# Kernel tuning notes

Measured on AMD Instinct MI355X. Metric: run time of the kernel, lower is better.

Reference implementation:

```python
import jax, jax.numpy as jnp
import numpy as np

B, IN, H = 4096, 1024, 1024


def setup_inputs() -> dict:
    key = jax.random.key(0)
    ks = jax.random.split(key, 16)
    s = 1.0 / np.sqrt(IN)
    inp = {
        "x_t": jax.random.normal(ks[0], (B, IN), jnp.float32),
        "h_prev": jax.random.normal(ks[1], (B, H), jnp.float32),
        "c_prev": jax.random.normal(ks[2], (B, H), jnp.float32),
        "W_xi": jax.random.uniform(ks[3], (H, IN), jnp.float32, -s, s),
        "W_hi": jax.random.normal(ks[4], (H, H), jnp.float32) / np.sqrt(H),
        "b_i": jnp.zeros((H,), jnp.float32),
        "W_xf": jax.random.uniform(ks[5], (H, IN), jnp.float32, -s, s),
        "W_hf": jax.random.normal(ks[6], (H, H), jnp.float32) / np.sqrt(H),
        "b_f": jnp.ones((H,), jnp.float32),
        "W_xg": jax.random.uniform(ks[7], (H, IN), jnp.float32, -s, s),
        "W_hg": jax.random.normal(ks[8], (H, H), jnp.float32) / np.sqrt(H),
        "b_g": jnp.zeros((H,), jnp.float32),
        "W_xo": jax.random.uniform(ks[9], (H, IN), jnp.float32, -s, s),
        "W_ho": jax.random.normal(ks[10], (H, H), jnp.float32) / np.sqrt(H),
        "b_o": jnp.zeros((H,), jnp.float32),
    }
    return inp


def reference(x_t, h_prev, c_prev,
              W_xi, W_hi, b_i,
              W_xf, W_hf, b_f,
              W_xg, W_hg, b_g,
              W_xo, W_ho, b_o):
    # i/f/g/o gates: sigmoid/sigmoid/tanh/sigmoid of (x W_x^T + h W_h^T + b)
    i_t = jax.nn.sigmoid(x_t @ W_xi.T + h_prev @ W_hi.T + b_i)
    f_t = jax.nn.sigmoid(x_t @ W_xf.T + h_prev @ W_hf.T + b_f)
    g_t = jnp.tanh(x_t @ W_xg.T + h_prev @ W_hg.T + b_g)
    o_t = jax.nn.sigmoid(x_t @ W_xo.T + h_prev @ W_ho.T + b_o)
    c_t = f_t * c_prev + i_t * g_t
    h_t = o_t * jnp.tanh(c_t)
    return (h_t, c_t)
```

## Files before the change

kernel.cpp:

```cpp
#include <hip/hip_runtime.h>
#include <hip/hip_bf16.h>


constexpr int Mdim = 4096;
constexpr int Ndim = 4096;
constexpr int Kdim = 2048;
constexpr int Hdim = 1024;
constexpr int BM = 256;
constexpr int BN = 256;
constexpr int BK = 64;
constexpr int NT = Kdim / BK;

using short8 = __attribute__((ext_vector_type(8))) short;
using f32x4  = __attribute__((ext_vector_type(4))) float;

__device__ __forceinline__ float sigmoid_(float x) {
    return 1.f / (1.f + __expf(-x));
}
__device__ __forceinline__ float tanh_(float x) {
    float e = __expf(2.f * x);
    return (e - 1.f) / (e + 1.f);
}

__global__ void build_A(const float* __restrict__ x, const float* __restrict__ h,
                        __hip_bfloat16* __restrict__ A) {
    int idx = blockIdx.x * 256 + threadIdx.x;
    int row = idx >> 8;
    int c8  = (idx & 255) * 8;
    const float* src = (c8 < 1024) ? (x + (size_t)row * 1024 + c8)
                                   : (h + (size_t)row * 1024 + (c8 - 1024));
    float4 f0 = ((const float4*)src)[0];
    float4 f1 = ((const float4*)src)[1];
    union { short8 v; __hip_bfloat16 e[8]; } u;
    u.e[0] = __float2bfloat16(f0.x); u.e[1] = __float2bfloat16(f0.y);
    u.e[2] = __float2bfloat16(f0.z); u.e[3] = __float2bfloat16(f0.w);
    u.e[4] = __float2bfloat16(f1.x); u.e[5] = __float2bfloat16(f1.y);
    u.e[6] = __float2bfloat16(f1.z); u.e[7] = __float2bfloat16(f1.w);
    *(short8*)(A + (size_t)row * Kdim + c8) = u.v;
}

__global__ void build_B(const float* __restrict__ Wxi, const float* __restrict__ Whi,
                        const float* __restrict__ Wxf, const float* __restrict__ Whf,
                        const float* __restrict__ Wxg, const float* __restrict__ Whg,
                        const float* __restrict__ Wxo, const float* __restrict__ Who,
                        __hip_bfloat16* __restrict__ B) {
    int idx = blockIdx.x * 256 + threadIdx.x;
    int n  = idx >> 8;
    int c8 = (idx & 255) * 8;
    int g = (n >> 4) & 3;
    int j = ((n >> 6) << 4) | (n & 15);
    const float* Wx = (g == 0) ? Wxi : (g == 1) ? Wxf : (g == 2) ? Wxg : Wxo;
    const float* Wh = (g == 0) ? Whi : (g == 1) ? Whf : (g == 2) ? Whg : Who;
    const float* src = (c8 < 1024) ? (Wx + (size_t)j * 1024 + c8)
                                   : (Wh + (size_t)j * 1024 + (c8 - 1024));
    float4 f0 = ((const float4*)src)[0];
    float4 f1 = ((const float4*)src)[1];
    union { short8 v; __hip_bfloat16 e[8]; } u;
    u.e[0] = __float2bfloat16(f0.x); u.e[1] = __float2bfloat16(f0.y);
    u.e[2] = __float2bfloat16(f0.z); u.e[3] = __float2bfloat16(f0.w);
    u.e[4] = __float2bfloat16(f1.x); u.e[5] = __float2bfloat16(f1.y);
    u.e[6] = __float2bfloat16(f1.z); u.e[7] = __float2bfloat16(f1.w);
    *(short8*)(B + (size_t)n * Kdim + c8) = u.v;
}

#define RD(p) (*(const short8*)(p))

__launch_bounds__(512, 1)
__global__ void lstm_gemm(const __hip_bfloat16* __restrict__ A,
                          const __hip_bfloat16* __restrict__ B,
                          const float* __restrict__ c_prev,
                          const float* __restrict__ b_i, const float* __restrict__ b_f,
                          const float* __restrict__ b_g, const float* __restrict__ b_o,
                          float* __restrict__ out_h, float* __restrict__ out_c) {
    __shared__ __hip_bfloat16 lds[2][2][2][128 * 64];

    const int tid  = threadIdx.x;
    const int lane = tid & 63;
    const int w    = tid >> 6;
    const int wr   = w >> 2;
    const int wc   = w & 3;
    const int l15  = lane & 15, lhi = lane >> 4;

    int bid = blockIdx.x;
    int swz = (bid & 7) * 32 + (bid >> 3);
    const int bm = (swz >> 4) * BM;
    const int bn = (swz & 15) * BN;

    const int srow_  = tid >> 3;
    const int schunk = ((tid & 7) ^ ((tid >> 3) & 7)) * 8;

    const int swz4 = (l15 & 7) << 4;
    const int kof0 = (lhi * 16) ^ swz4;
    const int kof1 = (64 + lhi * 16) ^ swz4;

#define STG1(dstbase, byteoff, srcptr, grow, kcol)                              \
    __builtin_amdgcn_global_load_lds(                                           \
        (const __attribute__((address_space(1))) unsigned*)(                    \
            (srcptr) + (size_t)((grow) + srow_) * Kdim + (kcol) + schunk),      \
        (__attribute__((address_space(3))) unsigned*)(                          \
            (char*)(dstbase) + (byteoff) + tid * 16), 16, 0, 0)

#define STAGE_TILE(s, kc)                                                       \
    do {                                                                        \
        STG1(&lds[s][1][0][0], 0,    B, bn + 0,   kc);                          \
        STG1(&lds[s][1][0][0], 8192, B, bn + 64,  kc);                          \
        STG1(&lds[s][1][1][0], 0,    B, bn + 128, kc);                          \
        STG1(&lds[s][1][1][0], 8192, B, bn + 192, kc);                          \
        STG1(&lds[s][0][0][0], 0,    A, bm + 0,   kc);                          \
        STG1(&lds[s][0][0][0], 8192, A, bm + 64,  kc);                          \
        STG1(&lds[s][0][1][0], 0,    A, bm + 128, kc);                          \
        STG1(&lds[s][0][1][0], 8192, A, bm + 192, kc);                          \
    } while (0)

    f32x4 acc[8][4];
#pragma unroll
    for (int a = 0; a < 8; ++a)
#pragma unroll
        for (int b = 0; b < 4; ++b)
            acc[a][b] = (f32x4){0.f, 0.f, 0.f, 0.f};

    STAGE_TILE(0, 0);
    __builtin_amdgcn_sched_barrier(0);
    asm volatile("s_waitcnt vmcnt(0)" ::: "memory");
    __builtin_amdgcn_s_barrier();

    for (int t = 0; t < NT; ++t) {
        const int d = t & 1;

        if (t + 1 < NT) STAGE_TILE(d ^ 1, (t + 1) * BK);

        const char* Ab = (const char*)&lds[d][0][wr][0] + l15 * 128;
        const char* Bb = (const char*)&lds[d][1][wc >> 1][0] + ((wc & 1) * 64 + l15) * 128;

        short8 af[8][2], bf[4][2];
#pragma unroll
        for (int a = 0; a < 8; ++a) {
            af[a][0] = RD(Ab + a * 2048 + kof0);
            af[a][1] = RD(Ab + a * 2048 + kof1);
        }
#pragma unroll
        for (int b = 0; b < 4; ++b) {
            bf[b][0] = RD(Bb + b * 2048 + kof0);
            bf[b][1] = RD(Bb + b * 2048 + kof1);
        }

        __builtin_amdgcn_s_setprio(1);
#pragma unroll
        for (int a = 0; a < 8; ++a)
#pragma unroll
            for (int b = 0; b < 4; ++b)
#pragma unroll
                for (int kk = 0; kk < 2; ++kk)
                    acc[a][b] = __builtin_amdgcn_mfma_f32_16x16x32_bf16(
                        af[a][kk], bf[b][kk], acc[a][b], 0, 0, 0);
        __builtin_amdgcn_s_setprio(0);

        if (t + 1 < NT) {
            __builtin_amdgcn_sched_barrier(0);
            asm volatile("s_waitcnt vmcnt(0) lgkmcnt(0)" ::: "memory");
            __builtin_amdgcn_s_barrier();
        }
    }
#undef STG1
#undef STAGE_TILE

    const int j0 = ((bn + wc * 64) >> 6) * 16 + l15;
    const float bi  = b_i[j0];
    const float bf_ = b_f[j0];
    const float bg  = b_g[j0];
    const float bo  = b_o[j0];

#pragma unroll
    for (int a = 0; a < 8; ++a) {
        int mbase = bm + wr * 128 + a * 16 + lhi * 4;
#pragma unroll
        for (int r = 0; r < 4; ++r) {
            int m = mbase + r;
            float vi = acc[a][0][r] + bi;
            float vf = acc[a][1][r] + bf_;
            float vg = acc[a][2][r] + bg;
            float vo = acc[a][3][r] + bo;
            float it = sigmoid_(vi);
            float ft = sigmoid_(vf);
            float gt = tanh_(vg);
            float ot = sigmoid_(vo);
            float cp = c_prev[(size_t)m * Hdim + j0];
            float ct = ft * cp + it * gt;
            float ht = ot * tanh_(ct);
            out_h[(size_t)m * Hdim + j0] = ht;
            out_c[(size_t)m * Hdim + j0] = ct;
        }
    }
}

extern "C" void kernel_launch(void* const* d_in, const int* in_sizes, int n_in,
                              void* d_out, int out_size, void* d_ws, size_t ws_size,
                              hipStream_t stream) {
    const float* x_t    = (const float*)d_in[0];
    const float* h_prev = (const float*)d_in[1];
    const float* c_prev = (const float*)d_in[2];
    const float* W_xi   = (const float*)d_in[3];
    const float* W_hi   = (const float*)d_in[4];
    const float* b_i    = (const float*)d_in[5];
    const float* W_xf   = (const float*)d_in[6];
    const float* W_hf   = (const float*)d_in[7];
    const float* b_f    = (const float*)d_in[8];
    const float* W_xg   = (const float*)d_in[9];
    const float* W_hg   = (const float*)d_in[10];
    const float* b_g    = (const float*)d_in[11];
    const float* W_xo   = (const float*)d_in[12];
    const float* W_ho   = (const float*)d_in[13];
    const float* b_o    = (const float*)d_in[14];

    float* out_h = (float*)d_out;
    float* out_c = out_h + (size_t)Mdim * Hdim;

    __hip_bfloat16* Abf = (__hip_bfloat16*)d_ws;
    __hip_bfloat16* Bbf = Abf + (size_t)Mdim * Kdim;

    build_A<<<4096, 256, 0, stream>>>(x_t, h_prev, Abf);
    build_B<<<4096, 256, 0, stream>>>(W_xi, W_hi, W_xf, W_hf, W_xg, W_hg, W_xo, W_ho, Bbf);

    lstm_gemm<<<dim3((Mdim / BM) * (Ndim / BN)), 512, 0, stream>>>(
        Abf, Bbf, c_prev, b_i, b_f, b_g, b_o, out_h, out_c);
}
```

Baseline: 86.34 us.

## Load B fragments directly from global into registers, halve LDS for two blocks/CU

```diff
diff --git a/kernel.cpp b/kernel.cpp
--- a/kernel.cpp
+++ b/kernel.cpp
@@ -65,14 +65,14 @@
 
 #define RD(p) (*(const short8*)(p))
 
-__launch_bounds__(512, 1)
+__launch_bounds__(512, 2)
 __global__ void lstm_gemm(const __hip_bfloat16* __restrict__ A,
                           const __hip_bfloat16* __restrict__ B,
                           const float* __restrict__ c_prev,
                           const float* __restrict__ b_i, const float* __restrict__ b_f,
                           const float* __restrict__ b_g, const float* __restrict__ b_o,
                           float* __restrict__ out_h, float* __restrict__ out_c) {
-    __shared__ __hip_bfloat16 lds[2][2][2][128 * 64];
+    __shared__ __hip_bfloat16 lds[2][2][128 * 64];
 
     const int tid  = threadIdx.x;
     const int lane = tid & 63;
@@ -93,23 +93,59 @@
     const int kof0 = (lhi * 16) ^ swz4;
     const int kof1 = (64 + lhi * 16) ^ swz4;
 
-#define STG1(dstbase, byteoff, srcptr, grow, kcol)                              \
+    const __hip_bfloat16* bRow = B + (size_t)(bn + wc * 64 + l15) * Kdim + lhi * 8;
+
+#define STG1(dstbase, byteoff, grow, kcol)                                      \
     __builtin_amdgcn_global_load_lds(                                           \
         (const __attribute__((address_space(1))) unsigned*)(                    \
-            (srcptr) + (size_t)((grow) + srow_) * Kdim + (kcol) + schunk),      \
+            A + (size_t)((grow) + srow_) * Kdim + (kcol) + schunk),             \
         (__attribute__((address_space(3))) unsigned*)(                          \
             (char*)(dstbase) + (byteoff) + tid * 16), 16, 0, 0)
 
-#define STAGE_TILE(s, kc)                                                       \
+#define STAGE_A(s, kc)                                                          \
     do {                                                                        \
-        STG1(&lds[s][1][0][0], 0,    B, bn + 0,   kc);                          \
-        STG1(&lds[s][1][0][0], 8192, B, bn + 64,  kc);                          \
-        STG1(&lds[s][1][1][0], 0,    B, bn + 128, kc);                          \
-        STG1(&lds[s][1][1][0], 8192, B, bn + 192, kc);                          \
-        STG1(&lds[s][0][0][0], 0,    A, bm + 0,   kc);                          \
-        STG1(&lds[s][0][0][0], 8192, A, bm + 64,  kc);                          \
-        STG1(&lds[s][0][1][0], 0,    A, bm + 128, kc);                          \
-        STG1(&lds[s][0][1][0], 8192, A, bm + 192, kc);                          \
+        STG1(&lds[s][0][0], 0,    bm + 0,   kc);                                \
+        STG1(&lds[s][0][0], 8192, bm + 64,  kc);                                \
+        STG1(&lds[s][1][0], 0,    bm + 128, kc);                                \
+        STG1(&lds[s][1][0], 8192, bm + 192, kc);                                \
+    } while (0)
+
+#define LOAD_B(dst, kt_)                                                        \
+    do {                                                                        \
+        _Pragma("unroll")                                                       \
+        for (int b_ = 0; b_ < 4; ++b_) {                                        \
+            dst[b_][0] = RD(bRow + (size_t)b_ * 16 * Kdim + (kt_));             \
+            dst[b_][1] = RD(bRow + (size_t)b_ * 16 * Kdim + (kt_) + 32);        \
+        }                                                                       \
+    } while (0)
+
+#define TILE_BODY(t_, dcur, BC, BN_)                                            \
+    do {                                                                        \
+        const int hasNext = (t_) + 1 < NT;                                      \
+        if (hasNext) {                                                          \
+            LOAD_B(BN_, ((t_) + 1) * BK);                                       \
+            STAGE_A(dcur ^ 1, ((t_) + 1) * BK);                                 \
+        }                                                                       \
+        const char* Ab = (const char*)&lds[dcur][wr][0] + l15 * 128;            \
+        __builtin_amdgcn_s_setprio(1);                                          \
+        _Pragma("unroll")                                                       \
+        for (int a = 0; a < 8; ++a) {                                           \
+            short8 af0 = RD(Ab + a * 2048 + kof0);                              \
+            short8 af1 = RD(Ab + a * 2048 + kof1);                              \
+            _Pragma("unroll")                                                   \
+            for (int b = 0; b < 4; ++b) {                                       \
+                acc[a][b] = __builtin_amdgcn_mfma_f32_16x16x32_bf16(            \
+                    af0, BC[b][0], acc[a][b], 0, 0, 0);                         \
+                acc[a][b] = __builtin_amdgcn_mfma_f32_16x16x32_bf16(            \
+                    af1, BC[b][1], acc[a][b], 0, 0, 0);                         \
+            }                                                                   \
+        }                                                                       \
+        __builtin_amdgcn_s_setprio(0);                                          \
+        if (hasNext) {                                                          \
+            __builtin_amdgcn_sched_barrier(0);                                  \
+            asm volatile("s_waitcnt vmcnt(0) lgkmcnt(0)" ::: "memory");         \
+            __builtin_amdgcn_s_barrier();                                       \
+        }                                                                       \
     } while (0)
 
     f32x4 acc[8][4];
@@ -119,50 +155,22 @@
         for (int b = 0; b < 4; ++b)
             acc[a][b] = (f32x4){0.f, 0.f, 0.f, 0.f};
 
-    STAGE_TILE(0, 0);
+    short8 bfA[4][2], bfB[4][2];
+
+    STAGE_A(0, 0);
+    LOAD_B(bfA, 0);
     __builtin_amdgcn_sched_barrier(0);
     asm volatile("s_waitcnt vmcnt(0)" ::: "memory");
     __builtin_amdgcn_s_barrier();
 
-    for (int t = 0; t < NT; ++t) {
-        const int d = t & 1;
-
-        if (t + 1 < NT) STAGE_TILE(d ^ 1, (t + 1) * BK);
-
-        const char* Ab = (const char*)&lds[d][0][wr][0] + l15 * 128;
-        const char* Bb = (const char*)&lds[d][1][wc >> 1][0] + ((wc & 1) * 64 + l15) * 128;
-
-        short8 af[8][2], bf[4][2];
-#pragma unroll
-        for (int a = 0; a < 8; ++a) {
-            af[a][0] = RD(Ab + a * 2048 + kof0);
-            af[a][1] = RD(Ab + a * 2048 + kof1);
-        }
-#pragma unroll
-        for (int b = 0; b < 4; ++b) {
-            bf[b][0] = RD(Bb + b * 2048 + kof0);
-            bf[b][1] = RD(Bb + b * 2048 + kof1);
-        }
-
-        __builtin_amdgcn_s_setprio(1);
-#pragma unroll
-        for (int a = 0; a < 8; ++a)
-#pragma unroll
-            for (int b = 0; b < 4; ++b)
-#pragma unroll
-                for (int kk = 0; kk < 2; ++kk)
-                    acc[a][b] = __builtin_amdgcn_mfma_f32_16x16x32_bf16(
-                        af[a][kk], bf[b][kk], acc[a][b], 0, 0, 0);
-        __builtin_amdgcn_s_setprio(0);
-
-        if (t + 1 < NT) {
-            __builtin_amdgcn_sched_barrier(0);
-            asm volatile("s_waitcnt vmcnt(0) lgkmcnt(0)" ::: "memory");
-            __builtin_amdgcn_s_barrier();
-        }
+    for (int tt = 0; tt < NT; tt += 2) {
+        TILE_BODY(tt,     0, bfA, bfB);
+        TILE_BODY(tt + 1, 1, bfB, bfA);
     }
 #undef STG1
-#undef STAGE_TILE
+#undef STAGE_A
+#undef LOAD_B
+#undef TILE_BODY
 
     const int j0 = ((bn + wc * 64) >> 6) * 16 + l15;
     const float bi  = b_i[j0];
```

After: 118.8 us. 37.6% more time.

## Shrink GEMM tile to 128x256, single-buffer LDS, raise occupancy to several blocks per CU

Applied to the files above, without the earlier changes.

```diff
diff --git a/kernel.cpp b/kernel.cpp
--- a/kernel.cpp
+++ b/kernel.cpp
@@ -6,7 +6,7 @@
 constexpr int Ndim = 4096;
 constexpr int Kdim = 2048;
 constexpr int Hdim = 1024;
-constexpr int BM = 256;
+constexpr int BM = 128;
 constexpr int BN = 256;
 constexpr int BK = 64;
 constexpr int NT = Kdim / BK;
@@ -65,14 +65,15 @@
 
 #define RD(p) (*(const short8*)(p))
 
-__launch_bounds__(512, 1)
+__launch_bounds__(512, 4)
 __global__ void lstm_gemm(const __hip_bfloat16* __restrict__ A,
                           const __hip_bfloat16* __restrict__ B,
                           const float* __restrict__ c_prev,
                           const float* __restrict__ b_i, const float* __restrict__ b_f,
                           const float* __restrict__ b_g, const float* __restrict__ b_o,
                           float* __restrict__ out_h, float* __restrict__ out_c) {
-    __shared__ __hip_bfloat16 lds[2][2][2][128 * 64];
+    __shared__ __hip_bfloat16 As[128 * 64];
+    __shared__ __hip_bfloat16 Bs[256 * 64];
 
     const int tid  = threadIdx.x;
     const int lane = tid & 63;
@@ -82,7 +83,7 @@
     const int l15  = lane & 15, lhi = lane >> 4;
 
     int bid = blockIdx.x;
-    int swz = (bid & 7) * 32 + (bid >> 3);
+    int swz = (bid & 7) * 64 + (bid >> 3);
     const int bm = (swz >> 4) * BM;
     const int bn = (swz & 15) * BN;
 
@@ -90,8 +91,6 @@
     const int schunk = ((tid & 7) ^ ((tid >> 3) & 7)) * 8;
 
     const int swz4 = (l15 & 7) << 4;
-    const int kof0 = (lhi * 16) ^ swz4;
-    const int kof1 = (64 + lhi * 16) ^ swz4;
 
 #define STG1(dstbase, byteoff, srcptr, grow, kcol)                              \
     __builtin_amdgcn_global_load_lds(                                           \
@@ -100,64 +99,54 @@
         (__attribute__((address_space(3))) unsigned*)(                          \
             (char*)(dstbase) + (byteoff) + tid * 16), 16, 0, 0)
 
-#define STAGE_TILE(s, kc)                                                       \
+#define STAGE_TILE(kc)                                                          \
     do {                                                                        \
-        STG1(&lds[s][1][0][0], 0,    B, bn + 0,   kc);                          \
-        STG1(&lds[s][1][0][0], 8192, B, bn + 64,  kc);                          \
-        STG1(&lds[s][1][1][0], 0,    B, bn + 128, kc);                          \
-        STG1(&lds[s][1][1][0], 8192, B, bn + 192, kc);                          \
-        STG1(&lds[s][0][0][0], 0,    A, bm + 0,   kc);                          \
-        STG1(&lds[s][0][0][0], 8192, A, bm + 64,  kc);                          \
-        STG1(&lds[s][0][1][0], 0,    A, bm + 128, kc);                          \
-        STG1(&lds[s][0][1][0], 8192, A, bm + 192, kc);                          \
+        STG1(As, 0,     A, bm + 0,   kc);                                       \
+        STG1(As, 8192,  A, bm + 64,  kc);                                       \
+        STG1(Bs, 0,     B, bn + 0,   kc);                                       \
+        STG1(Bs, 8192,  B, bn + 64,  kc);                                       \
+        STG1(Bs, 16384, B, bn + 128, kc);                                       \
+        STG1(Bs, 24576, B, bn + 192, kc);                                       \
     } while (0)
 
-    f32x4 acc[8][4];
-#pragma unroll
-    for (int a = 0; a < 8; ++a)
+    f32x4 acc[4][4];
+#pragma unroll
+    for (int a = 0; a < 4; ++a)
 #pragma unroll
         for (int b = 0; b < 4; ++b)
             acc[a][b] = (f32x4){0.f, 0.f, 0.f, 0.f};
 
-    STAGE_TILE(0, 0);
+    STAGE_TILE(0);
     __builtin_amdgcn_sched_barrier(0);
     asm volatile("s_waitcnt vmcnt(0)" ::: "memory");
     __builtin_amdgcn_s_barrier();
 
     for (int t = 0; t < NT; ++t) {
-        const int d = t & 1;
-
-        if (t + 1 < NT) STAGE_TILE(d ^ 1, (t + 1) * BK);
-
-        const char* Ab = (const char*)&lds[d][0][wr][0] + l15 * 128;
-        const char* Bb = (const char*)&lds[d][1][wc >> 1][0] + ((wc & 1) * 64 + l15) * 128;
-
-        short8 af[8][2], bf[4][2];
-#pragma unroll
-        for (int a = 0; a < 8; ++a) {
-            af[a][0] = RD(Ab + a * 2048 + kof0);
-            af[a][1] = RD(Ab + a * 2048 + kof1);
+#pragma unroll
+        for (int kk = 0; kk < 2; ++kk) {
+            const int kof = (kk * 64 + lhi * 16) ^ swz4;
+            short8 af[4], bf[4];
+#pragma unroll
+            for (int a = 0; a < 4; ++a)
+                af[a] = RD((const char*)As + (wr * 64 + a * 16 + l15) * 128 + kof);
+#pragma unroll
+            for (int b = 0; b < 4; ++b)
+                bf[b] = RD((const char*)Bs + (wc * 64 + b * 16 + l15) * 128 + kof);
+            __builtin_amdgcn_s_setprio(1);
+#pragma unroll
+            for (int a = 0; a < 4; ++a)
+#pragma unroll
+                for (int b = 0; b < 4; ++b)
+                    acc[a][b] = __builtin_amdgcn_mfma_f32_16x16x32_bf16(
+                        af[a], bf[b], acc[a][b], 0, 0, 0);
+            __builtin_amdgcn_s_setprio(0);
         }
-#pragma unroll
-        for (int b = 0; b < 4; ++b) {
-            bf[b][0] = RD(Bb + b * 2048 + kof0);
-            bf[b][1] = RD(Bb + b * 2048 + kof1);
-        }
-
-        __builtin_amdgcn_s_setprio(1);
-#pragma unroll
-        for (int a = 0; a < 8; ++a)
-#pragma unroll
-            for (int b = 0; b < 4; ++b)
-#pragma unroll
-                for (int kk = 0; kk < 2; ++kk)
-                    acc[a][b] = __builtin_amdgcn_mfma_f32_16x16x32_bf16(
-                        af[a][kk], bf[b][kk], acc[a][b], 0, 0, 0);
-        __builtin_amdgcn_s_setprio(0);
 
         if (t + 1 < NT) {
+            __builtin_amdgcn_s_barrier();
+            STAGE_TILE((t + 1) * BK);
             __builtin_amdgcn_sched_barrier(0);
-            asm volatile("s_waitcnt vmcnt(0) lgkmcnt(0)" ::: "memory");
+            asm volatile("s_waitcnt vmcnt(0)" ::: "memory");
             __builtin_amdgcn_s_barrier();
         }
     }
@@ -171,8 +160,8 @@
     const float bo  = b_o[j0];
 
 #pragma unroll
-    for (int a = 0; a < 8; ++a) {
-        int mbase = bm + wr * 128 + a * 16 + lhi * 4;
+    for (int a = 0; a < 4; ++a) {
+        int mbase = bm + wr * 64 + a * 16 + lhi * 4;
 #pragma unroll
         for (int r = 0; r < 4; ++r) {
             int m = mbase + r;
```

Result: no change. 87.20 us (+1.0%).
